# Optimization experiments

Measured on AMD Instinct MI355X. Metric: run time of the kernel, lower is better.

Reference implementation:

```python
import jax, jax.numpy as jnp
import numpy as np


def setup_inputs() -> dict:
    key = jax.random.key(0)
    ks = jax.random.split(key, 6)
    B, T = 512, 32768  # batch of audio segments, samples per segment
    return {
        "x": jax.random.normal(ks[0], (B, T), dtype=jnp.float32),
        "g": jax.random.normal(ks[1], (1,), dtype=jnp.float32),
        "r": jax.random.normal(ks[2], (1,), dtype=jnp.float32),
        "m_hp": jax.random.normal(ks[3], (1,), dtype=jnp.float32),
        "m_bp": jax.random.normal(ks[4], (1,), dtype=jnp.float32),
        "m_lp": jax.random.normal(ks[5], (1,), dtype=jnp.float32),
    }


def _biquad_coeffs(g, r, m_hp, m_bp, m_lp):
    # DSVF parameterization: g = tan(pi*sigmoid(g_raw)/2), r = softplus(r_raw)
    gg = jnp.tan(jnp.pi * jax.nn.sigmoid(g) / 2.0)
    rr = jax.nn.softplus(r)
    g2 = gg * gg
    b0 = g2 * m_lp + gg * m_bp + m_hp
    b1 = 2.0 * g2 * m_lp - 2.0 * m_hp
    b2 = g2 * m_lp - gg * m_bp + m_hp
    a0 = g2 + 2.0 * rr * gg + 1.0
    a1 = 2.0 * g2 - 2.0
    a2 = g2 - 2.0 * rr * gg + 1.0
    # scipy.signal.lfilter normalizes by a[0]
    inv_a0 = 1.0 / jnp.squeeze(a0)
    return (jnp.squeeze(b0) * inv_a0, jnp.squeeze(b1) * inv_a0,
            jnp.squeeze(b2) * inv_a0, jnppy_squeeze(a1) * inv_a0 if False else jnp.squeeze(a1) * inv_a0,
            jnp.squeeze(a2) * inv_a0)


def reference(x, g, r, m_hp, m_bp, m_lp):
    """Biquad IIR (direct form II transposed), zero initial state,
    matching scipy.signal.lfilter(b, a, x) along the last axis of x [B, T]."""
    b0, b1, b2, a1, a2 = _biquad_coeffs(g, r, m_hp, m_bp, m_lp)

    def step(carry, xt):  # xt: [B]
        z1, z2 = carry
        y = b0 * xt + z1
        z1n = b1 * xt - a1 * y + z2
        z2n = b2 * xt - a2 * y
        return (z1n, z2n), y

    B = x.shape[0]
    z0 = (jnp.zeros((B,), x.dtype), jnp.zeros((B,), x.dtype))
    _, y_t = jax.lax.scan(step, z0, x.T)  # scan over time: [T, B]
    return y_t.T  # [B, T]
```

## Files before the change

### kernel.cpp

```cpp
#include <hip/hip_runtime.h>
#include <math.h>


namespace {
constexpr int kT = 32768;
constexpr int kThreads = 512;
constexpr int kChunk = 64;
constexpr int kStride = kChunk + 1;
constexpr int kWaveLds = 64 * kStride;
constexpr int kSegQuads = 1024;
}

__device__ inline void coeffs_f32(const float* g, const float* r,
                                  const float* mhp, const float* mbp,
                                  const float* mlp, float& b0, float& b1,
                                  float& b2, float& a1, float& a2) {
  float graw = g[0], rraw = r[0];
  float sig = 1.0f / (1.0f + expf(-graw));
  float gg = tanf(1.5707963267948966f * sig);
  float rr = (rraw > 20.0f) ? rraw : log1pf(expf(rraw));
  float g2 = gg * gg;
  float m_hp = mhp[0], m_bp = mbp[0], m_lp = mlp[0];
  float B0 = g2 * m_lp + gg * m_bp + m_hp;
  float B1 = 2.0f * g2 * m_lp - 2.0f * m_hp;
  float B2 = g2 * m_lp - gg * m_bp + m_hp;
  float A0 = g2 + 2.0f * rr * gg + 1.0f;
  float A1 = 2.0f * g2 - 2.0f;
  float A2 = g2 - 2.0f * rr * gg + 1.0f;
  float inv = 1.0f / A0;
  b0 = B0 * inv; b1 = B1 * inv; b2 = B2 * inv;
  a1 = A1 * inv; a2 = A2 * inv;
}

#define IIR_STEP(xx, yy)                                         \
  do {                                                           \
    yy = fmaf(b0, xx, z1);                                       \
    z1 = fmaf(na1, yy, fmaf(b1, xx, z2));                        \
    z2 = fmaf(na2, yy, b2 * xx);                                 \
  } while (0)

#define MAT_SQ(w00, w01, w10, w11)                               \
  do {                                                           \
    double t00 = w00 * w00 + w01 * w10;                          \
    double t01 = w00 * w01 + w01 * w11;                          \
    double t10 = w10 * w00 + w11 * w10;                          \
    double t11 = w10 * w01 + w11 * w11;                          \
    w00 = t00; w01 = t01; w10 = t10; w11 = t11;                  \
  } while (0)

__global__ __launch_bounds__(kThreads) void k_fused(
    const float* __restrict__ x, const float* g, const float* r,
    const float* mhp, const float* mbp, const float* mlp,
    float* __restrict__ out) {
  __shared__ float xb[8 * kWaveLds];
  __shared__ double s1[kThreads], s2[kThreads];

  const int t = threadIdx.x;
  const int lane = t & 63;
  const int wave = t >> 6;
  const size_t rowoff = (size_t)blockIdx.x * kT;

  float b0, b1, b2, a1, a2;
  coeffs_f32(g, r, mhp, mbp, mlp, b0, b1, b2, a1, a2);
  float na1 = -a1, na2 = -a2;

  const float4* xv = (const float4*)(x + rowoff) + wave * kSegQuads;
  float* buf = &xb[wave * kWaveLds];
  float4 c[16];
#pragma unroll
  for (int i = 0; i < 16; ++i) c[i] = xv[i * 64 + lane];
#pragma unroll
  for (int i = 0; i < 16; ++i) {
    int f = i * 64 + lane;
    int base = (f >> 4) * kStride + ((f & 15) << 2);
    buf[base] = c[i].x; buf[base + 1] = c[i].y;
    buf[base + 2] = c[i].z; buf[base + 3] = c[i].w;
  }
  __syncthreads();
#pragma unroll
  for (int i = 0; i < 16; ++i) {
    int base = lane * kStride + (i << 2);
    c[i] = make_float4(buf[base], buf[base + 1], buf[base + 2], buf[base + 3]);
  }

  float z1 = 0.f, z2 = 0.f;
#pragma unroll
  for (int i = 0; i < 16; ++i) {
    float y;
    IIR_STEP(c[i].x, y); IIR_STEP(c[i].y, y);
    IIR_STEP(c[i].z, y); IIR_STEP(c[i].w, y);
  }

  double w00 = -(double)a1, w01 = 1.0, w10 = -(double)a2, w11 = 0.0;
#pragma unroll
  for (int i = 0; i < 6; ++i) MAT_SQ(w00, w01, w10, w11);

  double A0 = (double)z1, A1 = (double)z2;
  for (int o = 1; o < kThreads; o <<= 1) {
    s1[t] = A0; s2[t] = A1;
    __syncthreads();
    double q0 = 0.0, q1 = 0.0;
    if (t >= o) { q0 = s1[t - o]; q1 = s2[t - o]; }
    __syncthreads();
    A0 += w00 * q0 + w01 * q1;
    A1 += w10 * q0 + w11 * q1;
    MAT_SQ(w00, w01, w10, w11);
  }
  s1[t] = A0; s2[t] = A1;
  __syncthreads();
  double e0 = 0.0, e1 = 0.0;
  if (t > 0) { e0 = s1[t - 1]; e1 = s2[t - 1]; }

  z1 = (float)e0; z2 = (float)e1;
#pragma unroll
  for (int i = 0; i < 16; ++i) {
    float4 o4;
    IIR_STEP(c[i].x, o4.x); IIR_STEP(c[i].y, o4.y);
    IIR_STEP(c[i].z, o4.z); IIR_STEP(c[i].w, o4.w);
    c[i] = o4;
  }
#pragma unroll
  for (int i = 0; i < 16; ++i) {
    int base = lane * kStride + (i << 2);
    buf[base] = c[i].x; buf[base + 1] = c[i].y;
    buf[base + 2] = c[i].z; buf[base + 3] = c[i].w;
  }
  __syncthreads();

  float4* yv = (float4*)(out + rowoff) + wave * kSegQuads;
#pragma unroll
  for (int i = 0; i < 16; ++i) {
    int f = i * 64 + lane;
    int base = (f >> 4) * kStride + ((f & 15) << 2);
    yv[f] = make_float4(buf[base], buf[base + 1], buf[base + 2], buf[base + 3]);
  }
}

extern "C" void kernel_launch(void* const* d_in, const int* in_sizes, int n_in,
                              void* d_out, int out_size, void* d_ws,
                              size_t ws_size, hipStream_t stream) {
  const float* x   = (const float*)d_in[0];
  const float* g   = (const float*)d_in[1];
  const float* r   = (const float*)d_in[2];
  const float* mhp = (const float*)d_in[3];
  const float* mbp = (const float*)d_in[4];
  const float* mlp = (const float*)d_in[5];
  float* out = (float*)d_out;
  (void)d_ws; (void)ws_size;

  k_fused<<<512, kThreads, 0, stream>>>(x, g, r, mhp, mbp, mlp, out);
}
```

Baseline: 129.9 us.

## Load and store per-thread chunks directly instead of LDS transpose staging

Removes the shared-memory transpose used for coalesced global loads and stores. Each thread now reads and writes its own contiguous 64-float chunk with float4 accesses, so lanes touch addresses 256 bytes apart and the accesses are strided rather than coalesced. This drops about 130 KB of LDS per block and two barriers. It also adds a min-blocks hint to launch_bounds to raise occupancy. The risk is lower memory efficiency from the uncoalesced per-lane access pattern.

```diff
diff --git a/kernel.cpp b/kernel.cpp
--- a/kernel.cpp
+++ b/kernel.cpp
@@ -6,9 +6,6 @@
 constexpr int kT = 32768;
 constexpr int kThreads = 512;
 constexpr int kChunk = 64;
-constexpr int kStride = kChunk + 1;
-constexpr int kWaveLds = 64 * kStride;
-constexpr int kSegQuads = 1024;
 }
 
 __device__ inline void coeffs_f32(const float* g, const float* r,
@@ -48,40 +45,23 @@
     w00 = t00; w01 = t01; w10 = t10; w11 = t11;                  \
   } while (0)
 
-__global__ __launch_bounds__(kThreads) void k_fused(
+__global__ __launch_bounds__(kThreads, 4) void k_fused(
     const float* __restrict__ x, const float* g, const float* r,
     const float* mhp, const float* mbp, const float* mlp,
     float* __restrict__ out) {
-  __shared__ float xb[8 * kWaveLds];
   __shared__ double s1[kThreads], s2[kThreads];
 
   const int t = threadIdx.x;
-  const int lane = t & 63;
-  const int wave = t >> 6;
   const size_t rowoff = (size_t)blockIdx.x * kT;
 
   float b0, b1, b2, a1, a2;
   coeffs_f32(g, r, mhp, mbp, mlp, b0, b1, b2, a1, a2);
   float na1 = -a1, na2 = -a2;
 
-  const float4* xv = (const float4*)(x + rowoff) + wave * kSegQuads;
-  float* buf = &xb[wave * kWaveLds];
+  const float4* xq = (const float4*)(x + rowoff) + t * (kChunk / 4);
   float4 c[16];
 #pragma unroll
-  for (int i = 0; i < 16; ++i) c[i] = xv[i * 64 + lane];
-#pragma unroll
-  for (int i = 0; i < 16; ++i) {
-    int f = i * 64 + lane;
-    int base = (f >> 4) * kStride + ((f & 15) << 2);
-    buf[base] = c[i].x; buf[base + 1] = c[i].y;
-    buf[base + 2] = c[i].z; buf[base + 3] = c[i].w;
-  }
-  __syncthreads();
-#pragma unroll
-  for (int i = 0; i < 16; ++i) {
-    int base = lane * kStride + (i << 2);
-    c[i] = make_float4(buf[base], buf[base + 1], buf[base + 2], buf[base + 3]);
-  }
+  for (int i = 0; i < 16; ++i) c[i] = xq[i];
 
   float z1 = 0.f, z2 = 0.f;
 #pragma unroll
@@ -112,27 +92,13 @@
   if (t > 0) { e0 = s1[t - 1]; e1 = s2[t - 1]; }
 
   z1 = (float)e0; z2 = (float)e1;
+  float4* yq = (float4*)(out + rowoff) + t * (kChunk / 4);
 #pragma unroll
   for (int i = 0; i < 16; ++i) {
     float4 o4;
     IIR_STEP(c[i].x, o4.x); IIR_STEP(c[i].y, o4.y);
     IIR_STEP(c[i].z, o4.z); IIR_STEP(c[i].w, o4.w);
-    c[i] = o4;
-  }
-#pragma unroll
-  for (int i = 0; i < 16; ++i) {
-    int base = lane * kStride + (i << 2);
-    buf[base] = c[i].x; buf[base + 1] = c[i].y;
-    buf[base + 2] = c[i].z; buf[base + 3] = c[i].w;
-  }
-  __syncthreads();
-
-  float4* yv = (float4*)(out + rowoff) + wave * kSegQuads;
-#pragma unroll
-  for (int i = 0; i < 16; ++i) {
-    int f = i * 64 + lane;
-    int base = (f >> 4) * kStride + ((f & 15) << 2);
-    yv[f] = make_float4(buf[base], buf[base + 1], buf[base + 2], buf[base + 3]);
+    yq[i] = o4;
   }
 }
 
```

Measured after the change: 186.6 us. +43.6%, slower.
